# Performance work log

Measured on AMD Instinct MI355X. Metric: run time of the kernel, lower is better.

## Reference

```python
import jax, jax.numpy as jnp
import numpy as np
from jax import lax

jax.config.update("jax_enable_x64", True)  # source casts distances to double for sinkhorn

N_E = 512
E_DIM = 256
NUM_EXPERTS = 10
B = 8192
MU = 0.25
BETA = 1.0
SK_EPS = 0.01
SK_ITERS = 100


def setup_inputs() -> dict:
    key = jax.random.key(0)
    k0, k1, k2, k3 = jax.random.split(key, 4)
    x = jax.random.normal(k0, (B, E_DIM), dtype=jnp.float32)
    label = jax.random.randint(k1, (N_E,), 0, 10)  # cluster id per code of codebook 0
    gate_probs = jax.random.uniform(k2, (B, NUM_EXPERTS), dtype=jnp.float32)
    # embeddings initialized uniform(-1/n_e, 1/n_e) as in __init__
    emb = jax.random.uniform(k3, (NUM_EXPERTS + 1, N_E, E_DIM), dtype=jnp.float32,
                             minval=-1.0 / N_E, maxval=1.0 / N_E)
    return {"x": x, "label": label, "idx": 0, "gate_probs": gate_probs, "emb": emb}


def _sinkhorn(d, eps, iters):
    # standard SwAV-style sinkhorn (as used in UniTok/LETTER); d: [B, K] float64
    logits = -d / eps
    Q = jnp.exp(logits - jnp.max(logits))  # max-shift is a no-op after global normalization
    Q = (Q / jnp.sum(Q)).T  # [K, B]
    K, Bn = Q.shape

    def step(Q, _):
        Q = Q / (jnp.sum(Q, axis=1, keepdims=True) * K)
        Q = Q / (jnp.sum(Q, axis=0, keepdims=True) * Bn)
        return Q, None

    Q, _ = lax.scan(step, Q, None, length=iters)
    return (Q * Bn).T  # [B, K]


def _assign(latent, W):
    d = (jnp.sum(latent ** 2, axis=1, keepdims=True)
         + jnp.sum(W ** 2, axis=1)[None, :]
         - 2.0 * latent @ W.T)  # [B, n_e]
    mx, mn = jnp.max(d), jnp.min(d)
    mid = (mx + mn) / 2
    amp = mx - mid + 1e-5
    d = ((d - mid) / amp).astype(jnp.float64)
    Q = _sinkhorn(d, SK_EPS, SK_ITERS)
    return jnp.argmax(Q, axis=-1)  # [B]


def reference(x, label, idx, gate_probs, emb):
    latent = x.reshape(-1, E_DIM)  # [B, D]
    nb = latent.shape[0]

    # per-expert sinkhorn assignment (use_sk=True, sk_epsilon>0 path)
    indices_all = jax.vmap(lambda W: _assign(latent, W))(emb)          # [11, B]
    xq_all = jax.vmap(lambda W, i: W[i])(emb, indices_all)              # [11, B, D]

    x_q = jnp.einsum('be,ebd->bd', gate_probs, xq_all[:NUM_EXPERTS])
    x_q = 0.95 * x_q + 0.05 * xq_all[NUM_EXPERTS]

    # diversity loss on codebook 0: positive = another code in the same cluster
    ind0 = indices_all[0]                      # [B]
    clusters = label[ind0]                     # [B]
    ar = jnp.arange(N_E)
    pos_mask = (label[None, :] == clusters[:, None]) & (ar[None, :] != ind0[:, None])
    y_true = jnp.argmax(pos_mask, axis=1)      # deterministic positive sample
    sim = x_q @ emb[0].T                       # [B, n_e]
    sim = sim.at[jnp.arange(nb), ind0].add(-1e12)  # mask self-similarity
    logp = jax.nn.log_softmax(sim, axis=-1)
    diversity_loss = -jnp.mean(logp[jnp.arange(nb), y_true])

    commitment_loss = jnp.mean((lax.stop_gradient(x_q) - x) ** 2)
    codebook_loss = jnp.mean((x_q - lax.stop_gradient(x)) ** 2)
    loss = codebook_loss + MU * commitment_loss + BETA * diversity_loss

    # selected index per token: codebook of top expert
    expert_id = jnp.argmax(gate_probs, axis=1)          # [B] in [0,10)
    indices = indices_all.T[jnp.arange(nb), expert_id]  # [B]

    x_q_out = x + lax.stop_gradient(x_q - x)  # straight-through
    return x_q_out, loss, indices
```

## Files before the change

kernel.cpp:

```cpp
#include <hip/hip_runtime.h>
#include <cstdint>
#include <cstddef>

#define NTOK 8192
#define NE 512
#define EDIM 256
#define NEXPALL 11
#define NITER 100

static __device__ __forceinline__ double wredsum(double x) {
  for (int o = 32; o > 0; o >>= 1) x += __shfl_down(x, o, 64);
  return x;
}

static constexpr double S32 = 2.3283064365386963e-10;
static constexpr double Q32 = 4294967296.0;

__global__ void k_init(unsigned* colmin, double* r0, double* r1, double* uprev,
                       unsigned* dmaxA, unsigned* dminA, int* conv_iter, double* sums) {
  int i = blockIdx.x * 256 + threadIdx.x;
  if (i < NEXPALL * NTOK) colmin[i] = 0x7F800000u;
  if (i < NEXPALL * NE) { r0[i] = 0.0; r1[i] = 0.0; uprev[i] = 0.0; }
  if (i < NEXPALL) { dmaxA[i] = 0u; dminA[i] = 0x7F800000u; conv_iter[i] = 1 << 30; }
  if (i < 2) sums[i] = 0.0;
}

__global__ __launch_bounds__(256) void k_npsq(const float* __restrict__ p, float* __restrict__ o, int rows) {
  int r = blockIdx.x * 16 + (threadIdx.x >> 4);
  int l = threadIdx.x & 15;
  if (r >= rows) return;
  const float* a = p + (size_t)r * EDIM;
  int leaf = l >> 3;
  int j = l & 7;
  const float* base = a + leaf * 128 + j;
  float acc = __fmul_rn(base[0], base[0]);
#pragma unroll
  for (int i = 8; i < 128; i += 8) {
    float v = base[i];
    acc = __fadd_rn(acc, __fmul_rn(v, v));
  }
  acc = __fadd_rn(acc, __shfl_xor(acc, 1, 64));
  acc = __fadd_rn(acc, __shfl_xor(acc, 2, 64));
  acc = __fadd_rn(acc, __shfl_xor(acc, 4, 64));
  float other = __shfl_xor(acc, 8, 64);
  float tot = (leaf == 0) ? __fadd_rn(acc, other) : __fadd_rn(other, acc);
  if (l == 0) o[r] = tot;
}

__global__ __launch_bounds__(256) void k_gemm_d(const float* __restrict__ x, const float* __restrict__ emb,
                                                const float* __restrict__ sx, const float* __restrict__ sw,
                                                float* __restrict__ bigF,
                                                unsigned* __restrict__ colminA,
                                                unsigned* __restrict__ dmaxA,
                                                unsigned* __restrict__ dminA) {
  int bx = blockIdx.x, by = blockIdx.y, e = blockIdx.z;
  int tid = threadIdx.x;
  int tx = tid & 15, ty = tid >> 4;
  int b0 = bx * 64, k0 = by * 64;

  __shared__ float xs[64][17];
  __shared__ float es[64][17];
  __shared__ float sxs[64];
  __shared__ float sws[64];
  __shared__ unsigned colm[64];
  __shared__ float ttile[64][68];
  __shared__ float wrx[4], wrn[4];

  if (tid < 64) { sxs[tid] = sx[b0 + tid]; colm[tid] = 0x7F800000u; }
  else if (tid < 128) { sws[tid - 64] = sw[e * NE + k0 + tid - 64]; }

  float acc[4][4] = {};
  const float* xbase = x + (size_t)b0 * EDIM;
  const float* wbase = emb + ((size_t)e * NE + k0) * EDIM;
  int lr = tid >> 2;
  int lc = (tid & 3) * 4;

  for (int kc = 0; kc < EDIM; kc += 16) {
    float4 xv = *(const float4*)(xbase + (size_t)lr * EDIM + kc + lc);
    float4 wv = *(const float4*)(wbase + (size_t)lr * EDIM + kc + lc);
    __syncthreads();
    xs[lr][lc + 0] = xv.x; xs[lr][lc + 1] = xv.y; xs[lr][lc + 2] = xv.z; xs[lr][lc + 3] = xv.w;
    es[lr][lc + 0] = wv.x; es[lr][lc + 1] = wv.y; es[lr][lc + 2] = wv.z; es[lr][lc + 3] = wv.w;
    __syncthreads();
#pragma unroll
    for (int kk = 0; kk < 16; ++kk) {
      float a0 = xs[ty][kk], a1 = xs[ty + 16][kk], a2 = xs[ty + 32][kk], a3 = xs[ty + 48][kk];
      float w0 = es[tx][kk], w1 = es[tx + 16][kk], w2 = es[tx + 32][kk], w3 = es[tx + 48][kk];
      acc[0][0] = fmaf(a0, w0, acc[0][0]); acc[0][1] = fmaf(a0, w1, acc[0][1]);
      acc[0][2] = fmaf(a0, w2, acc[0][2]); acc[0][3] = fmaf(a0, w3, acc[0][3]);
      acc[1][0] = fmaf(a1, w0, acc[1][0]); acc[1][1] = fmaf(a1, w1, acc[1][1]);
      acc[1][2] = fmaf(a1, w2, acc[1][2]); acc[1][3] = fmaf(a1, w3, acc[1][3]);
      acc[2][0] = fmaf(a2, w0, acc[2][0]); acc[2][1] = fmaf(a2, w1, acc[2][1]);
      acc[2][2] = fmaf(a2, w2, acc[2][2]); acc[2][3] = fmaf(a2, w3, acc[2][3]);
      acc[3][0] = fmaf(a3, w0, acc[3][0]); acc[3][1] = fmaf(a3, w1, acc[3][1]);
      acc[3][2] = fmaf(a3, w2, acc[3][2]); acc[3][3] = fmaf(a3, w3, acc[3][3]);
    }
  }

  float dmx = -3.0e38f, dmn = 3.0e38f;
#pragma unroll
  for (int i = 0; i < 4; ++i) {
    float cmin = 3.0e38f;
#pragma unroll
    for (int j = 0; j < 4; ++j) {
      float m2 = __fmul_rn(2.0f, acc[i][j]);
      float dv = __fsub_rn(__fadd_rn(sxs[ty + 16 * i], sws[tx + 16 * j]), m2);
      ttile[tx + 16 * j][ty + 16 * i] = dv;
      dmx = fmaxf(dmx, dv); dmn = fminf(dmn, dv);
      cmin = fminf(cmin, dv);
    }
    atomicMin(&colm[ty + 16 * i], __float_as_uint(cmin));
  }
  for (int o = 32; o > 0; o >>= 1) {
    dmx = fmaxf(dmx, __shfl_down(dmx, o, 64));
    dmn = fminf(dmn, __shfl_down(dmn, o, 64));
  }
  int wv = tid >> 6, ln = tid & 63;
  if (ln == 0) { wrx[wv] = dmx; wrn[wv] = dmn; }
  __syncthreads();
  if (tid == 0) {
    float m1 = fmaxf(fmaxf(wrx[0], wrx[1]), fmaxf(wrx[2], wrx[3]));
    float m2 = fminf(fminf(wrn[0], wrn[1]), fminf(wrn[2], wrn[3]));
    atomicMax(dmaxA + e, __float_as_uint(m1));
    atomicMin(dminA + e, __float_as_uint(m2));
  }
  if (tid < 64) atomicMin(colminA + (size_t)e * NTOK + b0 + tid, colm[tid]);
  int orow = tid >> 2, oc = (tid & 3) << 4;
  float* ob = bigF + ((size_t)e * NE + k0 + orow) * NTOK + b0 + oc;
  *(float4*)(ob + 0) = *(float4*)&ttile[orow][oc + 0];
  *(float4*)(ob + 4) = *(float4*)&ttile[orow][oc + 4];
  *(float4*)(ob + 8) = *(float4*)&ttile[orow][oc + 8];
  *(float4*)(ob + 12) = *(float4*)&ttile[orow][oc + 12];
}

__global__ __launch_bounds__(256) void k_prep(const unsigned* __restrict__ colminA,
                                              const unsigned* __restrict__ dmaxA,
                                              const unsigned* __restrict__ dminA,
                                              double* __restrict__ cml, double* __restrict__ v) {
  int e = blockIdx.y;
  int b = blockIdx.x * 256 + threadIdx.x;
  float mx = __uint_as_float(dmaxA[e]);
  float mn = __uint_as_float(dminA[e]);
  float mid = __fmul_rn(__fadd_rn(mx, mn), 0.5f);
  float amp = __fadd_rn(__fsub_rn(mx, mid), 1e-5f);
  float cminf = __uint_as_float(colminA[(size_t)e * NTOK + b]);
  float dn = __fdiv_rn(__fsub_rn(cminf, mid), amp);
  double l = (-(double)dn) / 0.01;
  cml[(size_t)e * NTOK + b] = l;
  v[(size_t)e * NTOK + b] = exp(l);
}

__global__ __launch_bounds__(256) void k_build(float* __restrict__ bigF,
                                               const unsigned* __restrict__ dmaxA,
                                               const unsigned* __restrict__ dminA,
                                               const double* __restrict__ cml, const double* __restrict__ v0,
                                               double* __restrict__ r0) {
  int bx = blockIdx.x, k = blockIdx.y, e = blockIdx.z;
  int tid = threadIdx.x;
  float mx = __uint_as_float(dmaxA[e]);
  float mn = __uint_as_float(dminA[e]);
  float mid = __fmul_rn(__fadd_rn(mx, mn), 0.5f);
  float amp = __fadd_rn(__fsub_rn(mx, mid), 1e-5f);
  size_t rb = ((size_t)e * NE + k) * NTOK;
  int cb = bx * 2048 + tid * 8;
  float4 fa = *(const float4*)(bigF + rb + cb);
  float4 fb = *(const float4*)(bigF + rb + cb + 4);
  float din[8] = {fa.x, fa.y, fa.z, fa.w, fb.x, fb.y, fb.z, fb.w};
  unsigned qo[8];
  double racc = 0.0;
#pragma unroll
  for (int j = 0; j < 8; ++j) {
    int b = cb + j;
    float dn = __fdiv_rn(__fsub_rn(din[j], mid), amp);
    double l = (-(double)dn) / 0.01;
    double t = l - cml[(size_t)e * NTOK + b];
    double Bv = exp(t);
    double qd = (1.0 - Bv) * Q32;
    qd = fmin(fmax(qd, 0.0), 4294967295.0);
    unsigned q = (unsigned)llrint(qd);
    qo[j] = q;
    double Bq = fma(-(double)q, S32, 1.0);
    racc = fma(Bq, v0[(size_t)e * NTOK + b], racc);
  }
  uint4 oa = make_uint4(qo[0], qo[1], qo[2], qo[3]);
  uint4 ob2 = make_uint4(qo[4], qo[5], qo[6], qo[7]);
  *(uint4*)((unsigned*)bigF + rb + cb) = oa;
  *(uint4*)((unsigned*)bigF + rb + cb + 4) = ob2;
  racc = wredsum(racc);
  __shared__ double pr[4];
  int wv = tid >> 6, ln = tid & 63;
  if (ln == 0) pr[wv] = racc;
  __syncthreads();
  if (tid == 0) atomicAdd(&r0[e * NE + k], (pr[0] + pr[1]) + (pr[2] + pr[3]));
}

__global__ __launch_bounds__(256) void k_iter_a(const unsigned* __restrict__ bigU,
                                                const double* __restrict__ rc, double* __restrict__ rn,
                                                double* __restrict__ v, double* __restrict__ uprev,
                                                int* conv_iter, int t) {
  int e = blockIdx.y, bx = blockIdx.x, tid = threadIdx.x;
  int ci = ((volatile int*)conv_iter)[e];
  if (t > ci) {
    if (bx == 0) {
      int k2 = tid * 2;
      rn[e * NE + k2] = rc[e * NE + k2];
      rn[e * NE + k2 + 1] = rc[e * NE + k2 + 1];
    }
    return;
  }
  __shared__ double us[NE];
  __shared__ int okf;
  if (tid == 0) okf = 1;
  int k2 = tid * 2;
  double u0 = 1.0 / (512.0 * rc[e * NE + k2]);
  double u1 = 1.0 / (512.0 * rc[e * NE + k2 + 1]);
  us[k2] = u0; us[k2 + 1] = u1;
  __syncthreads();
  if (bx == 0) {
    double p0 = uprev[e * NE + k2], p1 = uprev[e * NE + k2 + 1];
    bool ok = (fabs(u0 - p0) <= 1e-13 * fabs(u0)) && (fabs(u1 - p1) <= 1e-13 * fabs(u1));
    if (!ok) okf = 0;
    uprev[e * NE + k2] = u0; uprev[e * NE + k2 + 1] = u1;
    rn[e * NE + k2] = 0.0; rn[e * NE + k2 + 1] = 0.0;
  }
  __syncthreads();
  if (bx == 0 && tid == 0 && okf) atomicMin(conv_iter + e, t);

  int col = bx * 256 + tid;
  const unsigned* cp = bigU + (size_t)e * NE * NTOK + col;
  double c0 = 0, c1 = 0, c2 = 0, c3 = 0;
#pragma unroll 2
  for (int k = 0; k < NE; k += 4) {
    unsigned q0 = cp[(size_t)(k + 0) * NTOK];
    unsigned q1 = cp[(size_t)(k + 1) * NTOK];
    unsigned q2 = cp[(size_t)(k + 2) * NTOK];
    unsigned q3 = cp[(size_t)(k + 3) * NTOK];
    c0 = fma(us[k + 0], fma(-(double)q0, S32, 1.0), c0);
    c1 = fma(us[k + 1], fma(-(double)q1, S32, 1.0), c1);
    c2 = fma(us[k + 2], fma(-(double)q2, S32, 1.0), c2);
    c3 = fma(us[k + 3], fma(-(double)q3, S32, 1.0), c3);
  }
  double c = (c0 + c1) + (c2 + c3);
  v[(size_t)e * NTOK + col] = 1.0 / (8192.0 * c);
}

__global__ __launch_bounds__(256) void k_iter_b(const unsigned* __restrict__ bigU,
                                                const double* __restrict__ v, double* __restrict__ rn,
                                                const int* conv_iter, int t) {
  int e = blockIdx.z;
  if (t > ((volatile int*)conv_iter)[e]) return;
  int bx = blockIdx.x, ky = blockIdx.y, tid = threadIdx.x;
  int wv = tid >> 6, ln = tid & 63;
  int cb = bx * 2048 + tid * 8;
  const double* vb = v + (size_t)e * NTOK + cb;
  double v0 = vb[0], v1 = vb[1], v2 = vb[2], v3 = vb[3];
  double v4 = vb[4], v5 = vb[5], v6 = vb[6], v7 = vb[7];
  __shared__ double part[16][4];
  size_t ebase = (size_t)e * NE * NTOK;
  for (int rr = 0; rr < 4; ++rr) {
#pragma unroll 4
    for (int kk = 0; kk < 16; ++kk) {
      int k = ky * 64 + rr * 16 + kk;
      const unsigned* rp = bigU + ebase + (size_t)k * NTOK + cb;
      uint4 qa = *(const uint4*)rp;
      uint4 qb = *(const uint4*)(rp + 4);
      double p;
      p = v0 * fma(-(double)qa.x, S32, 1.0);
      p = fma(v1, fma(-(double)qa.y, S32, 1.0), p);
      p = fma(v2, fma(-(double)qa.z, S32, 1.0), p);
      p = fma(v3, fma(-(double)qa.w, S32, 1.0), p);
      p = fma(v4, fma(-(double)qb.x, S32, 1.0), p);
      p = fma(v5, fma(-(double)qb.y, S32, 1.0), p);
      p = fma(v6, fma(-(double)qb.z, S32, 1.0), p);
      p = fma(v7, fma(-(double)qb.w, S32, 1.0), p);
      p = wredsum(p);
      if (ln == 0) part[kk][wv] = p;
    }
    __syncthreads();
    if (tid < 16)
      atomicAdd(&rn[e * NE + ky * 64 + rr * 16 + tid],
                (part[tid][0] + part[tid][1]) + (part[tid][2] + part[tid][3]));
    __syncthreads();
  }
}

__global__ __launch_bounds__(256) void k_final(const unsigned* __restrict__ bigU,
                                               const double* __restrict__ rfin, int* __restrict__ idxs) {
  int e = blockIdx.y, bx = blockIdx.x, tid = threadIdx.x;
  __shared__ double us[NE];
  int k2 = tid * 2;
  us[k2] = 1.0 / (512.0 * rfin[e * NE + k2]);
  us[k2 + 1] = 1.0 / (512.0 * rfin[e * NE + k2 + 1]);
  __syncthreads();
  int col = bx * 256 + tid;
  const unsigned* cp = bigU + (size_t)e * NE * NTOK + col;
  double best = -1.0;
  int bi = 0;
#pragma unroll 4
  for (int k = 0; k < NE; ++k) {
    double s = us[k] * fma(-(double)cp[(size_t)k * NTOK], S32, 1.0);
    if (s > best) { best = s; bi = k; }
  }
  idxs[(size_t)e * NTOK + col] = bi;
}

__global__ __launch_bounds__(256) void k_mix(const float* __restrict__ x, const float* __restrict__ gate,
                                             const float* __restrict__ emb, const int* __restrict__ idxs,
                                             float* __restrict__ xq, float* __restrict__ out0,
                                             float* __restrict__ outIdx, double* __restrict__ mse_sum) {
  int tid = threadIdx.x;
  int sub = tid >> 5, lane = tid & 31;
  int tok = blockIdx.x * 8 + sub;
  float acc[8] = {0, 0, 0, 0, 0, 0, 0, 0};
#pragma unroll
  for (int ee = 0; ee < 10; ++ee) {
    int id = idxs[(size_t)ee * NTOK + tok];
    float g = gate[tok * 10 + ee];
    const float* er = emb + ((size_t)ee * NE + id) * EDIM + lane;
#pragma unroll
    for (int dd = 0; dd < 8; ++dd) acc[dd] = fmaf(g, er[32 * dd], acc[dd]);
  }
  int id10 = idxs[(size_t)10 * NTOK + tok];
  const float* es = emb + ((size_t)10 * NE + id10) * EDIM + lane;
  double ms = 0.0;
#pragma unroll
  for (int dd = 0; dd < 8; ++dd) {
    int d = lane + 32 * dd;
    float q = 0.95f * acc[dd] + 0.05f * es[32 * dd];
    float xv = x[(size_t)tok * EDIM + d];
    float df = q - xv;
    out0[(size_t)tok * EDIM + d] = xv + df;
    xq[(size_t)tok * EDIM + d] = q;
    ms += (double)df * (double)df;
  }
  ms = wredsum(ms);
  __shared__ double pr[4];
  int wv = tid >> 6, ln = tid & 63;
  if (ln == 0) pr[wv] = ms;
  __syncthreads();
  if (tid == 0) atomicAdd(mse_sum, (pr[0] + pr[1]) + (pr[2] + pr[3]));
  if (lane == 0) {
    const float* gr = gate + tok * 10;
    float bg = gr[0];
    int be = 0;
#pragma unroll
    for (int ee = 1; ee < 10; ++ee) { float g = gr[ee]; if (g > bg) { bg = g; be = ee; } }
    outIdx[tok] = (float)idxs[(size_t)be * NTOK + tok];
  }
}

__global__ __launch_bounds__(256) void k_simgemm(const float* __restrict__ xq, const float* __restrict__ emb,
                                                 float* __restrict__ sim) {
  int bx = blockIdx.x, by = blockIdx.y, tid = threadIdx.x;
  int tx = tid & 15, ty = tid >> 4;
  int b0 = bx * 64, j0 = by * 64;
  __shared__ float xs[64][17];
  __shared__ float es[64][17];
  __shared__ float tt[64][68];
  float acc[4][4] = {};
  int lr = tid >> 2, lc = (tid & 3) * 4;
  for (int kc = 0; kc < EDIM; kc += 16) {
    float4 xv = *(const float4*)(xq + (size_t)(b0 + lr) * EDIM + kc + lc);
    float4 ev = *(const float4*)(emb + (size_t)(j0 + lr) * EDIM + kc + lc);
    __syncthreads();
    xs[lr][lc + 0] = xv.x; xs[lr][lc + 1] = xv.y; xs[lr][lc + 2] = xv.z; xs[lr][lc + 3] = xv.w;
    es[lr][lc + 0] = ev.x; es[lr][lc + 1] = ev.y; es[lr][lc + 2] = ev.z; es[lr][lc + 3] = ev.w;
    __syncthreads();
#pragma unroll
    for (int kk = 0; kk < 16; ++kk) {
      float a0 = xs[ty][kk], a1 = xs[ty + 16][kk], a2 = xs[ty + 32][kk], a3 = xs[ty + 48][kk];
      float w0 = es[tx][kk], w1 = es[tx + 16][kk], w2 = es[tx + 32][kk], w3 = es[tx + 48][kk];
      acc[0][0] = fmaf(a0, w0, acc[0][0]); acc[0][1] = fmaf(a0, w1, acc[0][1]);
      acc[0][2] = fmaf(a0, w2, acc[0][2]); acc[0][3] = fmaf(a0, w3, acc[0][3]);
      acc[1][0] = fmaf(a1, w0, acc[1][0]); acc[1][1] = fmaf(a1, w1, acc[1][1]);
      acc[1][2] = fmaf(a1, w2, acc[1][2]); acc[1][3] = fmaf(a1, w3, acc[1][3]);
      acc[2][0] = fmaf(a2, w0, acc[2][0]); acc[2][1] = fmaf(a2, w1, acc[2][1]);
      acc[2][2] = fmaf(a2, w2, acc[2][2]); acc[2][3] = fmaf(a2, w3, acc[2][3]);
      acc[3][0] = fmaf(a3, w0, acc[3][0]); acc[3][1] = fmaf(a3, w1, acc[3][1]);
      acc[3][2] = fmaf(a3, w2, acc[3][2]); acc[3][3] = fmaf(a3, w3, acc[3][3]);
    }
  }
#pragma unroll
  for (int i = 0; i < 4; ++i)
#pragma unroll
    for (int j = 0; j < 4; ++j) tt[ty + 16 * i][tx + 16 * j] = acc[i][j];
  __syncthreads();
  int orow = tid >> 2, oc = (tid & 3) << 4;
  float* ob = sim + (size_t)(b0 + orow) * NE + j0 + oc;
  *(float4*)(ob + 0) = *(float4*)&tt[orow][oc + 0];
  *(float4*)(ob + 4) = *(float4*)&tt[orow][oc + 4];
  *(float4*)(ob + 8) = *(float4*)&tt[orow][oc + 8];
  *(float4*)(ob + 12) = *(float4*)&tt[orow][oc + 12];
}

__global__ __launch_bounds__(256) void k_div(const float* __restrict__ sim, const int* __restrict__ idxs,
                                             const int* __restrict__ label, double* __restrict__ div_sum) {
  __shared__ int lab[NE];
  int tid = threadIdx.x;
  lab[tid] = label[tid];
  lab[256 + tid] = label[256 + tid];
  __syncthreads();
  int wv = tid >> 6, ln = tid & 63;
  int b = blockIdx.x * 4 + wv;
  int ind0 = idxs[b];
  int clu = lab[ind0];
  const float* sr = sim + (size_t)b * NE;
  double vals[8];
  double mx = -1e300;
  int ys = 1024;
#pragma unroll
  for (int c = 0; c < 8; ++c) {
    int j = ln + 64 * c;
    double vv = (double)sr[j];
    if (j == ind0) vv -= 1e12;
    vals[c] = vv;
    mx = fmax(mx, vv);
    if (lab[j] == clu && j != ind0 && j < ys) ys = j;
  }
  for (int o = 32; o > 0; o >>= 1) {
    mx = fmax(mx, __shfl_xor(mx, o, 64));
    ys = min(ys, __shfl_xor(ys, o, 64));
  }
  int y = (ys >= 1024) ? 0 : ys;
  double se = 0.0, vy = 0.0;
#pragma unroll
  for (int c = 0; c < 8; ++c) {
    int j = ln + 64 * c;
    se += exp(vals[c] - mx);
    if (j == y) vy = vals[c];
  }
  for (int o = 32; o > 0; o >>= 1) {
    se += __shfl_xor(se, o, 64);
    vy += __shfl_xor(vy, o, 64);
  }
  if (ln == 0) {
    double lse = mx + log(se);
    atomicAdd(div_sum, lse - vy);
  }
}

__global__ void k_loss(const double* __restrict__ sums, float* __restrict__ out) {
  double mse = sums[0] / 2097152.0;
  double dv = sums[1] / 8192.0;
  double loss = (mse + 0.25 * mse) + dv;
  out[0] = (float)loss;
}

extern "C" void kernel_launch(void* const* d_in, const int* in_sizes, int n_in,
                              void* d_out, int out_size, void* d_ws, size_t ws_size,
                              hipStream_t stream) {
  (void)in_sizes; (void)n_in; (void)out_size;
  const float* x = (const float*)d_in[0];
  const int* label = (const int*)d_in[1];
  const float* gate = (const float*)d_in[3];
  const float* emb = (const float*)d_in[4];
  float* out = (float*)d_out;
  float* out0 = out;
  float* outLoss = out + (size_t)NTOK * EDIM;
  float* outIdx = out + (size_t)NTOK * EDIM + 1;

  char* w = (char*)d_ws;
  size_t off = 0;
  auto alloc = [&](size_t bytes) -> void* {
    void* p = w + off;
    off += (bytes + 15) & ~(size_t)15;
    return p;
  };
  float* bigF = (float*)alloc((size_t)NEXPALL * NE * NTOK * 4);
  unsigned* bigU = (unsigned*)bigF;
  float* sim = (float*)bigF;
  unsigned* colminA = (unsigned*)alloc((size_t)NEXPALL * NTOK * 4);
  double* cml = (double*)alloc((size_t)NEXPALL * NTOK * 8);
  double* v = (double*)alloc((size_t)NEXPALL * NTOK * 8);
  double* r0 = (double*)alloc((size_t)NEXPALL * NE * 8);
  double* r1 = (double*)alloc((size_t)NEXPALL * NE * 8);
  double* uprev = (double*)alloc((size_t)NEXPALL * NE * 8);
  float* sxF = (float*)alloc((size_t)NTOK * 4);
  float* swF = (float*)alloc((size_t)NEXPALL * NE * 4);
  unsigned* dmaxA = (unsigned*)alloc(NEXPALL * 4);
  unsigned* dminA = (unsigned*)alloc(NEXPALL * 4);
  int* conv_iter = (int*)alloc(NEXPALL * 4);
  int* idxs = (int*)alloc((size_t)NEXPALL * NTOK * 4);
  float* xq = (float*)alloc((size_t)NTOK * EDIM * 4);
  double* sums = (double*)alloc(2 * 8);
  if (off > ws_size) return;

  k_init<<<352, 256, 0, stream>>>(colminA, r0, r1, uprev, dmaxA, dminA, conv_iter, sums);
  k_npsq<<<NTOK / 16, 256, 0, stream>>>(x, sxF, NTOK);
  k_npsq<<<(NEXPALL * NE) / 16, 256, 0, stream>>>(emb, swF, NEXPALL * NE);
  k_gemm_d<<<dim3(128, 8, NEXPALL), 256, 0, stream>>>(x, emb, sxF, swF, bigF, colminA, dmaxA, dminA);
  k_prep<<<dim3(32, NEXPALL), 256, 0, stream>>>(colminA, dmaxA, dminA, cml, v);
  k_build<<<dim3(4, NE, NEXPALL), 256, 0, stream>>>(bigF, dmaxA, dminA, cml, v, r0);
  for (int t = 1; t <= NITER; ++t) {
    const double* rc = (t & 1) ? r0 : r1;
    double* rn = (t & 1) ? r1 : r0;
    k_iter_a<<<dim3(32, NEXPALL), 256, 0, stream>>>(bigU, rc, rn, v, uprev, conv_iter, t);
    k_iter_b<<<dim3(4, 8, NEXPALL), 256, 0, stream>>>(bigU, v, rn, conv_iter, t);
  }
  k_final<<<dim3(32, NEXPALL), 256, 0, stream>>>(bigU, r1, idxs);
  k_mix<<<NTOK / 8, 256, 0, stream>>>(x, gate, emb, idxs, xq, out0, outIdx, sums);
  k_simgemm<<<dim3(128, 8), 256, 0, stream>>>(xq, emb, sim);
  k_div<<<NTOK / 4, 256, 0, stream>>>(sim, idxs, label, sums + 1);
  k_loss<<<1, 1, 0, stream>>>(sums, outLoss);
}
```

Before: 1.519 ms.

## Enlarge GEMM tiles to 128x128 with 8x8 register blocking and prefetch

Both FP32 GEMM kernels (distance and similarity) move from 64x64 tiles with 4x4 per-thread outputs to 128x128 tiles with 8x8 outputs. Shared memory is laid out k-major so the inner loop reads float4 vectors. Global loads for the next k-chunk are issued before the current chunk's compute. The distance kernel now writes its output straight from registers instead of through a shared transpose tile. This raises arithmetic intensity and cuts shared-memory traffic, at the cost of more registers, fewer blocks, and possibly less efficient strided global stores.

```diff
diff --git a/kernel.cpp b/kernel.cpp
--- a/kernel.cpp
+++ b/kernel.cpp
@@ -47,76 +47,95 @@
   if (l == 0) o[r] = tot;
 }
 
-__global__ __launch_bounds__(256) void k_gemm_d(const float* __restrict__ x, const float* __restrict__ emb,
-                                                const float* __restrict__ sx, const float* __restrict__ sw,
-                                                float* __restrict__ bigF,
-                                                unsigned* __restrict__ colminA,
-                                                unsigned* __restrict__ dmaxA,
-                                                unsigned* __restrict__ dminA) {
+__global__ __launch_bounds__(256, 2) void k_gemm_d(const float* __restrict__ x, const float* __restrict__ emb,
+                                                   const float* __restrict__ sx, const float* __restrict__ sw,
+                                                   float* __restrict__ bigF,
+                                                   unsigned* __restrict__ colminA,
+                                                   unsigned* __restrict__ dmaxA,
+                                                   unsigned* __restrict__ dminA) {
   int bx = blockIdx.x, by = blockIdx.y, e = blockIdx.z;
   int tid = threadIdx.x;
   int tx = tid & 15, ty = tid >> 4;
-  int b0 = bx * 64, k0 = by * 64;
-
-  __shared__ float xs[64][17];
-  __shared__ float es[64][17];
-  __shared__ float sxs[64];
-  __shared__ float sws[64];
-  __shared__ unsigned colm[64];
-  __shared__ float ttile[64][68];
+  int b0 = bx * 128, k0 = by * 128;
+
+  __shared__ float xs[16][128];
+  __shared__ float es[16][128];
+  __shared__ float sxs[128];
+  __shared__ float sws[128];
+  __shared__ unsigned colm[128];
   __shared__ float wrx[4], wrn[4];
 
-  if (tid < 64) { sxs[tid] = sx[b0 + tid]; colm[tid] = 0x7F800000u; }
-  else if (tid < 128) { sws[tid - 64] = sw[e * NE + k0 + tid - 64]; }
-
-  float acc[4][4] = {};
-  const float* xbase = x + (size_t)b0 * EDIM;
-  const float* wbase = emb + ((size_t)e * NE + k0) * EDIM;
-  int lr = tid >> 2;
-  int lc = (tid & 3) * 4;
+  if (tid < 128) { sxs[tid] = sx[b0 + tid]; colm[tid] = 0x7F800000u; }
+  else { sws[tid - 128] = sw[e * NE + k0 + tid - 128]; }
+
+  int lr = tid & 127;
+  int lh = tid >> 7;
+  const float* xrow = x + (size_t)(b0 + lr) * EDIM + lh * 8;
+  const float* wrow = emb + ((size_t)e * NE + k0 + lr) * EDIM + lh * 8;
+
+  float4 xa = *(const float4*)(xrow + 0);
+  float4 xb = *(const float4*)(xrow + 4);
+  float4 wa = *(const float4*)(wrow + 0);
+  float4 wb = *(const float4*)(wrow + 4);
+
+  float acc[8][8] = {};
 
   for (int kc = 0; kc < EDIM; kc += 16) {
-    float4 xv = *(const float4*)(xbase + (size_t)lr * EDIM + kc + lc);
-    float4 wv = *(const float4*)(wbase + (size_t)lr * EDIM + kc + lc);
     __syncthreads();
-    xs[lr][lc + 0] = xv.x; xs[lr][lc + 1] = xv.y; xs[lr][lc + 2] = xv.z; xs[lr][lc + 3] = xv.w;
-    es[lr][lc + 0] = wv.x; es[lr][lc + 1] = wv.y; es[lr][lc + 2] = wv.z; es[lr][lc + 3] = wv.w;
+    xs[lh * 8 + 0][lr] = xa.x; xs[lh * 8 + 1][lr] = xa.y;
+    xs[lh * 8 + 2][lr] = xa.z; xs[lh * 8 + 3][lr] = xa.w;
+    xs[lh * 8 + 4][lr] = xb.x; xs[lh * 8 + 5][lr] = xb.y;
+    xs[lh * 8 + 6][lr] = xb.z; xs[lh * 8 + 7][lr] = xb.w;
+    es[lh * 8 + 0][lr] = wa.x; es[lh * 8 + 1][lr] = wa.y;
+    es[lh * 8 + 2][lr] = wa.z; es[lh * 8 + 3][lr] = wa.w;
+    es[lh * 8 + 4][lr] = wb.x; es[lh * 8 + 5][lr] = wb.y;
+    es[lh * 8 + 6][lr] = wb.z; es[lh * 8 + 7][lr] = wb.w;
     __syncthreads();
+    if (kc + 16 < EDIM) {
+      xa = *(const float4*)(xrow + kc + 16);
+      xb = *(const float4*)(xrow + kc + 20);
+      wa = *(const float4*)(wrow + kc + 16);
+      wb = *(const float4*)(wrow + kc + 20);
+    }
 #pragma unroll
     for (int kk = 0; kk < 16; ++kk) {
-      float a0 = xs[ty][kk], a1 = xs[ty + 16][kk], a2 = xs[ty + 32][kk], a3 = xs[ty + 48][kk];
-      float w0 = es[tx][kk], w1 = es[tx + 16][kk], w2 = es[tx + 32][kk], w3 = es[tx + 48][kk];
-      acc[0][0] = fmaf(a0, w0, acc[0][0]); acc[0][1] = fmaf(a0, w1, acc[0][1]);
-      acc[0][2] = fmaf(a0, w2, acc[0][2]); acc[0][3] = fmaf(a0, w3, acc[0][3]);
-      acc[1][0] = fmaf(a1, w0, acc[1][0]); acc[1][1] = fmaf(a1, w1, acc[1][1]);
-      acc[1][2] = fmaf(a1, w2, acc[1][2]); acc[1][3] = fmaf(a1, w3, acc[1][3]);
-      acc[2][0] = fmaf(a2, w0, acc[2][0]); acc[2][1] = fmaf(a2, w1, acc[2][1]);
-      acc[2][2] = fmaf(a2, w2, acc[2][2]); acc[2][3] = fmaf(a2, w3, acc[2][3]);
-      acc[3][0] = fmaf(a3, w0, acc[3][0]); acc[3][1] = fmaf(a3, w1, acc[3][1]);
-      acc[3][2] = fmaf(a3, w2, acc[3][2]); acc[3][3] = fmaf(a3, w3, acc[3][3]);
+      float4 xv0 = *(const float4*)&xs[kk][tx * 4];
+      float4 xv1 = *(const float4*)&xs[kk][64 + tx * 4];
+      float4 wv0 = *(const float4*)&es[kk][ty * 4];
+      float4 wv1 = *(const float4*)&es[kk][64 + ty * 4];
+      float xr[8] = {xv0.x, xv0.y, xv0.z, xv0.w, xv1.x, xv1.y, xv1.z, xv1.w};
+      float wr[8] = {wv0.x, wv0.y, wv0.z, wv0.w, wv1.x, wv1.y, wv1.z, wv1.w};
+#pragma unroll
+      for (int i = 0; i < 8; ++i)
+#pragma unroll
+        for (int j = 0; j < 8; ++j)
+          acc[i][j] = fmaf(xr[i], wr[j], acc[i][j]);
     }
   }
 
   float dmx = -3.0e38f, dmn = 3.0e38f;
 #pragma unroll
-  for (int i = 0; i < 4; ++i) {
+  for (int i = 0; i < 8; ++i) {
+    int tokL = (i >> 2) * 64 + tx * 4 + (i & 3);
+    float sxv = sxs[tokL];
     float cmin = 3.0e38f;
 #pragma unroll
-    for (int j = 0; j < 4; ++j) {
+    for (int j = 0; j < 8; ++j) {
+      int codeL = (j >> 2) * 64 + ty * 4 + (j & 3);
       float m2 = __fmul_rn(2.0f, acc[i][j]);
-      float dv = __fsub_rn(__fadd_rn(sxs[ty + 16 * i], sws[tx + 16 * j]), m2);
-      ttile[tx + 16 * j][ty + 16 * i] = dv;
+      float dv = __fsub_rn(__fadd_rn(sxv, sws[codeL]), m2);
+      acc[i][j] = dv;
       dmx = fmaxf(dmx, dv); dmn = fminf(dmn, dv);
       cmin = fminf(cmin, dv);
     }
-    atomicMin(&colm[ty + 16 * i], __float_as_uint(cmin));
+    atomicMin(&colm[tokL], __float_as_uint(cmin));
   }
   for (int o = 32; o > 0; o >>= 1) {
     dmx = fmaxf(dmx, __shfl_down(dmx, o, 64));
     dmn = fminf(dmn, __shfl_down(dmn, o, 64));
   }
-  int wv = tid >> 6, ln = tid & 63;
-  if (ln == 0) { wrx[wv] = dmx; wrn[wv] = dmn; }
+  int wvi = tid >> 6, ln = tid & 63;
+  if (ln == 0) { wrx[wvi] = dmx; wrn[wvi] = dmn; }
   __syncthreads();
   if (tid == 0) {
     float m1 = fmaxf(fmaxf(wrx[0], wrx[1]), fmaxf(wrx[2], wrx[3]));
@@ -124,13 +143,19 @@
     atomicMax(dmaxA + e, __float_as_uint(m1));
     atomicMin(dminA + e, __float_as_uint(m2));
   }
-  if (tid < 64) atomicMin(colminA + (size_t)e * NTOK + b0 + tid, colm[tid]);
-  int orow = tid >> 2, oc = (tid & 3) << 4;
-  float* ob = bigF + ((size_t)e * NE + k0 + orow) * NTOK + b0 + oc;
-  *(float4*)(ob + 0) = *(float4*)&ttile[orow][oc + 0];
-  *(float4*)(ob + 4) = *(float4*)&ttile[orow][oc + 4];
-  *(float4*)(ob + 8) = *(float4*)&ttile[orow][oc + 8];
-  *(float4*)(ob + 12) = *(float4*)&ttile[orow][oc + 12];
+  if (tid < 128) atomicMin(colminA + (size_t)e * NTOK + b0 + tid, colm[tid]);
+#pragma unroll
+  for (int j2 = 0; j2 < 2; ++j2)
+#pragma unroll
+    for (int cc = 0; cc < 4; ++cc) {
+      int code = j2 * 64 + ty * 4 + cc;
+      int cj = j2 * 4 + cc;
+      float* ob = bigF + ((size_t)e * NE + k0 + code) * NTOK + b0;
+      float4 lo = make_float4(acc[0][cj], acc[1][cj], acc[2][cj], acc[3][cj]);
+      float4 hi = make_float4(acc[4][cj], acc[5][cj], acc[6][cj], acc[7][cj]);
+      *(float4*)(ob + tx * 4) = lo;
+      *(float4*)(ob + 64 + tx * 4) = hi;
+    }
 }
 
 __global__ __launch_bounds__(256) void k_prep(const unsigned* __restrict__ colminA,
@@ -349,48 +374,63 @@
   }
 }
 
-__global__ __launch_bounds__(256) void k_simgemm(const float* __restrict__ xq, const float* __restrict__ emb,
-                                                 float* __restrict__ sim) {
+__global__ __launch_bounds__(256, 2) void k_simgemm(const float* __restrict__ xq, const float* __restrict__ emb,
+                                                    float* __restrict__ sim) {
   int bx = blockIdx.x, by = blockIdx.y, tid = threadIdx.x;
   int tx = tid & 15, ty = tid >> 4;
-  int b0 = bx * 64, j0 = by * 64;
-  __shared__ float xs[64][17];
-  __shared__ float es[64][17];
-  __shared__ float tt[64][68];
-  float acc[4][4] = {};
-  int lr = tid >> 2, lc = (tid & 3) * 4;
+  int b0 = bx * 128, j0 = by * 128;
+  __shared__ float xs[16][128];
+  __shared__ float es[16][128];
+  int lr = tid & 127;
+  int lh = tid >> 7;
+  const float* xrow = xq + (size_t)(b0 + lr) * EDIM + lh * 8;
+  const float* erow = emb + (size_t)(j0 + lr) * EDIM + lh * 8;
+  float4 xa = *(const float4*)(xrow + 0);
+  float4 xb = *(const float4*)(xrow + 4);
+  float4 wa = *(const float4*)(erow + 0);
+  float4 wb = *(const float4*)(erow + 4);
+  float acc[8][8] = {};
   for (int kc = 0; kc < EDIM; kc += 16) {
-    float4 xv = *(const float4*)(xq + (size_t)(b0 + lr) * EDIM + kc + lc);
-    float4 ev = *(const float4*)(emb + (size_t)(j0 + lr) * EDIM + kc + lc);
     __syncthreads();
-    xs[lr][lc + 0] = xv.x; xs[lr][lc + 1] = xv.y; xs[lr][lc + 2] = xv.z; xs[lr][lc + 3] = xv.w;
-    es[lr][lc + 0] = ev.x; es[lr][lc + 1] = ev.y; es[lr][lc + 2] = ev.z; es[lr][lc + 3] = ev.w;
+    xs[lh * 8 + 0][lr] = xa.x; xs[lh * 8 + 1][lr] = xa.y;
+    xs[lh * 8 + 2][lr] = xa.z; xs[lh * 8 + 3][lr] = xa.w;
+    xs[lh * 8 + 4][lr] = xb.x; xs[lh * 8 + 5][lr] = xb.y;
+    xs[lh * 8 + 6][lr] = xb.z; xs[lh * 8 + 7][lr] = xb.w;
+    es[lh * 8 + 0][lr] = wa.x; es[lh * 8 + 1][lr] = wa.y;
+    es[lh * 8 + 2][lr] = wa.z; es[lh * 8 + 3][lr] = wa.w;
+    es[lh * 8 + 4][lr] = wb.x; es[lh * 8 + 5][lr] = wb.y;
+    es[lh * 8 + 6][lr] = wb.z; es[lh * 8 + 7][lr] = wb.w;
     __syncthreads();
+    if (kc + 16 < EDIM) {
+      xa = *(const float4*)(xrow + kc + 16);
+      xb = *(const float4*)(xrow + kc + 20);
+      wa = *(const float4*)(erow + kc + 16);
+      wb = *(const float4*)(erow + kc + 20);
+    }
 #pragma unroll
     for (int kk = 0; kk < 16; ++kk) {
-      float a0 = xs[ty][kk], a1 = xs[ty + 16][kk], a2 = xs[ty + 32][kk], a3 = xs[ty + 48][kk];
-      float w0 = es[tx][kk], w1 = es[tx + 16][kk], w2 = es[tx + 32][kk], w3 = es[tx + 48][kk];
-      acc[0][0] = fmaf(a0, w0, acc[0][0]); acc[0][1] = fmaf(a0, w1, acc[0][1]);
-      acc[0][2] = fmaf(a0, w2, acc[0][2]); acc[0][3] = fmaf(a0, w3, acc[0][3]);
-      acc[1][0] = fmaf(a1, w0, acc[1][0]); acc[1][1] = fmaf(a1, w1, acc[1][1]);
-      acc[1][2] = fmaf(a1, w2, acc[1][2]); acc[1][3] = fmaf(a1, w3, acc[1][3]);
-      acc[2][0] = fmaf(a2, w0, acc[2][0]); acc[2][1] = fmaf(a2, w1, acc[2][1]);
-      acc[2][2] = fmaf(a2, w2, acc[2][2]); acc[2][3] = fmaf(a2, w3, acc[2][3]);
-      acc[3][0] = fmaf(a3, w0, acc[3][0]); acc[3][1] = fmaf(a3, w1, acc[3][1]);
-      acc[3][2] = fmaf(a3, w2, acc[3][2]); acc[3][3] = fmaf(a3, w3, acc[3][3]);
-    }
-  }
-#pragma unroll
-  for (int i = 0; i < 4; ++i)
-#pragma unroll
-    for (int j = 0; j < 4; ++j) tt[ty + 16 * i][tx + 16 * j] = acc[i][j];
-  __syncthreads();
-  int orow = tid >> 2, oc = (tid & 3) << 4;
-  float* ob = sim + (size_t)(b0 + orow) * NE + j0 + oc;
-  *(float4*)(ob + 0) = *(float4*)&tt[orow][oc + 0];
-  *(float4*)(ob + 4) = *(float4*)&tt[orow][oc + 4];
-  *(float4*)(ob + 8) = *(float4*)&tt[orow][oc + 8];
-  *(float4*)(ob + 12) = *(float4*)&tt[orow][oc + 12];
+      float4 xv0 = *(const float4*)&xs[kk][ty * 4];
+      float4 xv1 = *(const float4*)&xs[kk][64 + ty * 4];
+      float4 wv0 = *(const float4*)&es[kk][tx * 4];
+      float4 wv1 = *(const float4*)&es[kk][64 + tx * 4];
+      float xr[8] = {xv0.x, xv0.y, xv0.z, xv0.w, xv1.x, xv1.y, xv1.z, xv1.w};
+      float wr[8] = {wv0.x, wv0.y, wv0.z, wv0.w, wv1.x, wv1.y, wv1.z, wv1.w};
+#pragma unroll
+      for (int i = 0; i < 8; ++i)
+#pragma unroll
+        for (int j = 0; j < 8; ++j)
+          acc[i][j] = fmaf(xr[i], wr[j], acc[i][j]);
+    }
+  }
+#pragma unroll
+  for (int i = 0; i < 8; ++i) {
+    int tok = (i >> 2) * 64 + ty * 4 + (i & 3);
+    float* ob = sim + (size_t)(b0 + tok) * NE + j0;
+    float4 lo = make_float4(acc[i][0], acc[i][1], acc[i][2], acc[i][3]);
+    float4 hi = make_float4(acc[i][4], acc[i][5], acc[i][6], acc[i][7]);
+    *(float4*)(ob + tx * 4) = lo;
+    *(float4*)(ob + 64 + tx * 4) = hi;
+  }
 }
 
 __global__ __launch_bounds__(256) void k_div(const float* __restrict__ sim, const int* __restrict__ idxs,
@@ -488,7 +528,7 @@
   k_init<<<352, 256, 0, stream>>>(colminA, r0, r1, uprev, dmaxA, dminA, conv_iter, sums);
   k_npsq<<<NTOK / 16, 256, 0, stream>>>(x, sxF, NTOK);
   k_npsq<<<(NEXPALL * NE) / 16, 256, 0, stream>>>(emb, swF, NEXPALL * NE);
-  k_gemm_d<<<dim3(128, 8, NEXPALL), 256, 0, stream>>>(x, emb, sxF, swF, bigF, colminA, dmaxA, dminA);
+  k_gemm_d<<<dim3(64, 4, NEXPALL), 256, 0, stream>>>(x, emb, sxF, swF, bigF, colminA, dmaxA, dminA);
   k_prep<<<dim3(32, NEXPALL), 256, 0, stream>>>(colminA, dmaxA, dminA, cml, v);
   k_build<<<dim3(4, NE, NEXPALL), 256, 0, stream>>>(bigF, dmaxA, dminA, cml, v, r0);
   for (int t = 1; t <= NITER; ++t) {
@@ -499,7 +539,7 @@
   }
   k_final<<<dim3(32, NEXPALL), 256, 0, stream>>>(bigU, r1, idxs);
   k_mix<<<NTOK / 8, 256, 0, stream>>>(x, gate, emb, idxs, xq, out0, outIdx, sums);
-  k_simgemm<<<dim3(128, 8), 256, 0, stream>>>(xq, emb, sim);
+  k_simgemm<<<dim3(64, 4), 256, 0, stream>>>(xq, emb, sim);
   k_div<<<NTOK / 4, 256, 0, stream>>>(sim, idxs, label, sums + 1);
   k_loss<<<1, 1, 0, stream>>>(sums, outLoss);
 }
```

Measured after the change: 1.341 ms. 11.7% less time.
